# Kernel optimization log

Measured on AMD Instinct MI355X. Metric: run time of the kernel, lower is better.

## Reference

```python
import jax, jax.numpy as jnp
import numpy as np

N_NODES = 100000
N_EDGES = 800000
IN_FEATS = 128
NUM_CLASSES = 64


def setup_inputs() -> dict:
    key = jax.random.key(0)
    k1, k2, k3, k4 = jax.random.split(key, 4)
    x = jax.random.normal(k1, (N_NODES, IN_FEATS), dtype=jnp.float32)
    edge_src = jax.random.randint(k2, (N_EDGES,), 0, N_NODES, dtype=jnp.int64)
    edge_dst = jax.random.randint(k3, (N_EDGES,), 0, N_NODES, dtype=jnp.int64)
    W_neigh = jax.random.normal(k4, (NUM_CLASSES, IN_FEATS), dtype=jnp.float32) * (1.0 / np.sqrt(IN_FEATS))
    b_neigh = jnp.zeros((NUM_CLASSES,), dtype=jnp.float32)
    return {"x": x, "edge_src": edge_src, "edge_dst": edge_dst,
            "W_neigh": W_neigh, "b_neigh": b_neigh}


def reference(x, edge_src, edge_dst, W_neigh, b_neigh):
    # DGL SAGEConv with aggregator_type='gcn':
    #   h_neigh[v] = (sum_{u->v} x[u] + x[v]) / (in_degree(v) + 1)
    #   out = h_neigh @ W_neigh^T + b_neigh
    n = x.shape[0]
    # gather source features per edge, scatter-sum into destinations
    neigh_sum = jax.ops.segment_sum(x[edge_src], edge_dst, num_segments=n)  # [N, F]
    deg = jax.ops.segment_sum(jnp.ones((edge_src.shape[0],), dtype=x.dtype),
                              edge_dst, num_segments=n)                     # [N]
    h = (neigh_sum + x) / (deg + 1.0)[:, None]
    out = jnp.einsum('nf,cf->nc', h, W_neigh) + b_neigh
    return out
```

## Files before the change

### kernel.cpp

```cpp
#include <hip/hip_runtime.h>

#define N_NODES 100000
#define N_EDGES 800000
#define IN_FEATS 128
#define NUM_CLASSES 64

#define NSB    98
#define SCAP   9216
#define BINCAP 56
#define NBKT   12500
#define NBKT_PAD (NSB * 128)
#define HCAP   88
#define BKCAP  176

#define K1_GRID 1955

typedef short bf16x8 __attribute__((ext_vector_type(8)));
typedef float f32x4  __attribute__((ext_vector_type(4)));

static __device__ __forceinline__ unsigned short f2bf(float f) {
    unsigned u = __float_as_uint(f);
    unsigned r = (u + 0x7fffu + ((u >> 16) & 1u)) >> 16;
    return (unsigned short)r;
}
static __device__ __forceinline__ float bf2f(unsigned short v) {
    return __uint_as_float(((unsigned)v) << 16);
}

static __device__ __forceinline__ void gemm_body(char* smem, int gid,
                                                 const float* __restrict__ x,
                                                 const float* __restrict__ W,
                                                 unsigned short* __restrict__ y16) {
    const long base = (long)gid * 64;
    if (base >= N_NODES) return;

    unsigned short* Wf = (unsigned short*)smem;
    typedef unsigned short XsRow[136];
    XsRow* Xs = (XsRow*)(smem + 16384);

    const int tid = threadIdx.x;

    for (int i = tid; i < 4 * 4 * 64 * 8; i += 256) {
        const int j    = i & 7;
        const int lane = (i >> 3) & 63;
        const int t    = (i >> 9) & 3;
        const int s    = i >> 11;
        const int k = s * 32 + ((lane >> 4) << 3) + j;
        const int c = t * 16 + (lane & 15);
        Wf[i] = f2bf(W[c * IN_FEATS + k]);
    }

#pragma unroll
    for (int it = 0; it < 8; ++it) {
        const int i   = tid + it * 256;
        const int row = i >> 5;
        const int c4  = (i & 31) << 2;
        const long node = base + row;
        float4 v = make_float4(0.f, 0.f, 0.f, 0.f);
        if (node < N_NODES) v = *(const float4*)&x[node * IN_FEATS + c4];
        ushort4 w4;
        w4.x = f2bf(v.x); w4.y = f2bf(v.y); w4.z = f2bf(v.z); w4.w = f2bf(v.w);
        *(ushort4*)&Xs[row][c4] = w4;
    }
    __syncthreads();

    const int wave = tid >> 6;
    const int lane = tid & 63;
    const long nb  = base + wave * 16;

    bf16x8 wf[4][4];
#pragma unroll
    for (int s = 0; s < 4; ++s)
#pragma unroll
        for (int t = 0; t < 4; ++t)
            wf[s][t] = *(const bf16x8*)&Wf[(((s * 4 + t) * 64) + lane) * 8];

    f32x4 acc[4];
#pragma unroll
    for (int t = 0; t < 4; ++t) acc[t] = (f32x4){0.f, 0.f, 0.f, 0.f};

    const int m  = lane & 15;
    const int kq = lane >> 4;
    const unsigned short* arow = &Xs[wave * 16 + m][kq * 8];

#pragma unroll
    for (int s = 0; s < 4; ++s) {
        bf16x8 af = *(const bf16x8*)(arow + s * 32);
#pragma unroll
        for (int t = 0; t < 4; ++t)
            acc[t] = __builtin_amdgcn_mfma_f32_16x16x32_bf16(af, wf[s][t], acc[t], 0, 0, 0);
    }

    const int ccol  = lane & 15;
    const int rbase = (lane >> 4) << 2;
#pragma unroll
    for (int t = 0; t < 4; ++t) {
#pragma unroll
        for (int r = 0; r < 4; ++r) {
            const long n2 = nb + rbase + r;
            if (n2 < N_NODES)
                y16[n2 * NUM_CLASSES + t * 16 + ccol] = f2bf(acc[t][r]);
        }
    }
}

static __device__ __forceinline__ void p1_body(char* smem, int p1id,
                                               const int* __restrict__ esrc,
                                               const int* __restrict__ edst,
                                               int* __restrict__ sbcur,
                                               unsigned* __restrict__ stage) {
    typedef unsigned BinRow[BINCAP];
    BinRow* bins = (BinRow*)smem;
    int* bcnt  = (int*)(smem + 21952);
    int* bbase = (int*)(smem + 21952 + 392);

    const int tid = threadIdx.x;
    for (int i = tid; i < NSB; i += 256) bcnt[i] = 0;
    __syncthreads();

    const int e0 = p1id * 2048;
#pragma unroll
    for (int it = 0; it < 8; ++it) {
        const int e = e0 + it * 256 + tid;
        if (e < N_EDGES) {
            const unsigned s  = (unsigned)esrc[e];
            const unsigned d  = (unsigned)edst[e];
            const unsigned sb = d >> 10;
            const unsigned pk = s | ((d & 1023u) << 17);
            const int p = atomicAdd(&bcnt[sb], 1);
            if (p < BINCAP) {
                bins[sb][p] = pk;
            } else {
                const int gp = atomicAdd(&sbcur[sb << 4], 1);
                if (gp < SCAP) stage[sb * SCAP + gp] = pk;
            }
        }
    }
    __syncthreads();

    if (tid < NSB) {
        const int c = min(bcnt[tid], BINCAP);
        bcnt[tid]  = c;
        bbase[tid] = atomicAdd(&sbcur[tid << 4], c);
    }
    __syncthreads();

    for (int i = tid; i < NSB * BINCAP; i += 256) {
        const int sb = i / BINCAP;
        const int k  = i - sb * BINCAP;
        if (k < bcnt[sb]) {
            const int pos = bbase[sb] + k;
            if (pos < SCAP) stage[sb * SCAP + pos] = bins[sb][k];
        }
    }
}

__global__ __launch_bounds__(256) void k1_gemm_scatter(const float* __restrict__ x,
                                                       const float* __restrict__ W,
                                                       unsigned short* __restrict__ y16,
                                                       const int* __restrict__ esrc,
                                                       const int* __restrict__ edst,
                                                       int* __restrict__ sbcur,
                                                       unsigned* __restrict__ stage) {
    __shared__ __align__(16) char smem[33792];
    const int bid = blockIdx.x;
    const int r   = bid % 5;
    if (r == 4) {
        p1_body(smem, bid / 5, esrc, edst, sbcur, stage);
    } else {
        gemm_body(smem, (bid / 5) * 4 + r, x, W, y16);
    }
}

__global__ __launch_bounds__(256) void scatter_p2(const unsigned* __restrict__ stage,
                                                  const int* __restrict__ sbcur,
                                                  unsigned* __restrict__ pairs,
                                                  int* __restrict__ cnt_g) {
    __shared__ int lcnt[128];
    const int sb  = blockIdx.x >> 1;
    const int h   = blockIdx.x & 1;
    const int tid = threadIdx.x;

    if (tid < 128) lcnt[tid] = 0;
    __syncthreads();

    const int ecnt = min(sbcur[sb << 4], SCAP);
    const int half = (ecnt + 1) >> 1;
    const int lo   = h * half;
    const int hi   = min(ecnt, lo + half);

    const unsigned* sp = stage + (size_t)sb * SCAP;
    unsigned* pp = pairs + (size_t)sb * 128 * BKCAP + h * HCAP;

    for (int i = lo + tid; i < hi; i += 256) {
        const unsigned pk   = sp[i];
        const unsigned dlow = pk >> 17;
        const int fb = (int)(dlow >> 3);
        const unsigned dl = dlow & 7u;
        const int r = atomicAdd(&lcnt[fb], 1);
        if (r < HCAP) pp[fb * BKCAP + r] = (pk & 0x1FFFFu) | (dl << 20);
    }
    __syncthreads();

    if (tid < 128) cnt_g[((sb << 7) + tid) * 2 + h] = min(lcnt[tid], HCAP);
}

__global__ __launch_bounds__(256) void gather_bucket(const unsigned short* __restrict__ y16,
                                                     const unsigned* __restrict__ pairs,
                                                     const int* __restrict__ cnt_g,
                                                     const float* __restrict__ b,
                                                     float* __restrict__ out) {
    __shared__ float slab[4][8][64];
    __shared__ int   cnt[4][8];

    const int tid  = threadIdx.x;
    const int wave = tid >> 6;
    const int lane = tid & 63;
    const int bkt  = blockIdx.x;

    {
        float4* sz = (float4*)&slab[0][0][0];
        sz[tid]       = make_float4(0.f, 0.f, 0.f, 0.f);
        sz[tid + 256] = make_float4(0.f, 0.f, 0.f, 0.f);
    }

    const int half = wave >> 1;
    const int ws   = wave & 1;
    const int mh = cnt_g[bkt * 2 + half];
    const int q  = (mh + 1) >> 1;
    const int s0 = ws * q;
    const int s1 = min(mh, s0 + q);
    const int m  = max(0, s1 - s0);

    const unsigned* pb = pairs + (size_t)bkt * BKCAP + half * HCAP + s0;
    unsigned pr = 0;
    if (lane < m) pr = pb[lane];

    unsigned long long cnt64 = 0;
    __syncthreads();

    int j = 0;
    for (; j + 4 <= m; j += 4) {
        const unsigned p0 = __shfl(pr, j);
        const unsigned p1 = __shfl(pr, j + 1);
        const unsigned p2 = __shfl(pr, j + 2);
        const unsigned p3 = __shfl(pr, j + 3);
        const float v0 = bf2f(y16[(size_t)(p0 & 0xFFFFFu) * NUM_CLASSES + lane]);
        const float v1 = bf2f(y16[(size_t)(p1 & 0xFFFFFu) * NUM_CLASSES + lane]);
        const float v2 = bf2f(y16[(size_t)(p2 & 0xFFFFFu) * NUM_CLASSES + lane]);
        const float v3 = bf2f(y16[(size_t)(p3 & 0xFFFFFu) * NUM_CLASSES + lane]);
        slab[wave][p0 >> 20][lane] += v0;
        slab[wave][p1 >> 20][lane] += v1;
        slab[wave][p2 >> 20][lane] += v2;
        slab[wave][p3 >> 20][lane] += v3;
        cnt64 += (1ull << ((p0 >> 20) * 8)) + (1ull << ((p1 >> 20) * 8))
               + (1ull << ((p2 >> 20) * 8)) + (1ull << ((p3 >> 20) * 8));
    }
    for (; j < m; ++j) {
        const unsigned p = __shfl(pr, j);
        slab[wave][p >> 20][lane] += bf2f(y16[(size_t)(p & 0xFFFFFu) * NUM_CLASSES + lane]);
        cnt64 += 1ull << ((p >> 20) * 8);
    }

    if (lane < 8) cnt[wave][lane] = (int)((cnt64 >> (lane * 8)) & 0xFFull);
    __syncthreads();

    const int c = tid & 63;
#pragma unroll
    for (int i = 0; i < 2; ++i) {
        const int n = (tid >> 6) + 4 * i;
        const size_t v = ((size_t)bkt << 3) + n;
        const float s = slab[0][n][c] + slab[1][n][c] + slab[2][n][c] + slab[3][n][c];
        const int  dg = cnt[0][n] + cnt[1][n] + cnt[2][n] + cnt[3][n];
        const float self = bf2f(y16[v * NUM_CLASSES + c]);
        out[v * NUM_CLASSES + c] = (s + self) / (float)(dg + 1) + b[c];
    }
}

extern "C" void kernel_launch(void* const* d_in, const int* in_sizes, int n_in,
                              void* d_out, int out_size, void* d_ws, size_t ws_size,
                              hipStream_t stream) {
    const float* x    = (const float*)d_in[0];
    const int*   esrc = (const int*)d_in[1];
    const int*   edst = (const int*)d_in[2];
    const float* W    = (const float*)d_in[3];
    const float* b    = (const float*)d_in[4];
    float* out = (float*)d_out;

    char* p = (char*)d_ws;
    unsigned short* y16 = (unsigned short*)p;  p += (size_t)N_NODES * NUM_CLASSES * 2;
    unsigned* stage     = (unsigned*)p;        p += (size_t)NSB * SCAP * 4;
    unsigned* pairs     = (unsigned*)p;        p += (size_t)NBKT * BKCAP * 4;
    int* cnt_g          = (int*)p;             p += (size_t)NBKT_PAD * 2 * 4;
    int* sbcur          = (int*)p;             p += (size_t)NSB * 16 * 4;

    hipMemsetAsync(sbcur, 0, (size_t)NSB * 16 * 4, stream);

    k1_gemm_scatter<<<K1_GRID, 256, 0, stream>>>(x, W, y16, esrc, edst, sbcur, stage);

    scatter_p2<<<NSB * 2, 256, 0, stream>>>(stage, sbcur, pairs, cnt_g);

    gather_bucket<<<NBKT, 256, 0, stream>>>(y16, pairs, cnt_g, b, out);
}
```

Before: 156.0 us.

## Sort edges by destination node within buckets and gather per node with registers

The second scatter pass becomes a count-then-place counting sort. Edges within each 8-node bucket are grouped by exact destination node, with per-node counts and offsets, and the grid grows to four blocks per superblock. The gather kernel now gives one wave per bucket and accumulates each node's neighbours in registers using readlane indices. This removes the shared-memory slab accumulation, the barriers and the packed degree counters. The cost is that scatter_p2 reads the stage buffer twice, and any bucket with more than 128 edges is silently truncated.

```diff
diff --git a/kernel.cpp b/kernel.cpp
--- a/kernel.cpp
+++ b/kernel.cpp
@@ -10,8 +10,7 @@
 #define BINCAP 56
 #define NBKT   12500
 #define NBKT_PAD (NSB * 128)
-#define HCAP   88
-#define BKCAP  176
+#define PB_CAP 128
 
 #define K1_GRID 1955
 
@@ -176,104 +175,97 @@
                                                   const int* __restrict__ sbcur,
                                                   unsigned* __restrict__ pairs,
                                                   int* __restrict__ cnt_g) {
-    __shared__ int lcnt[128];
-    const int sb  = blockIdx.x >> 1;
-    const int h   = blockIdx.x & 1;
+    __shared__ int lcnt[256];
+    __shared__ int loff[256];
+    const int sb  = blockIdx.x >> 2;
+    const int q   = blockIdx.x & 3;
     const int tid = threadIdx.x;
 
-    if (tid < 128) lcnt[tid] = 0;
+    lcnt[tid] = 0;
     __syncthreads();
 
     const int ecnt = min(sbcur[sb << 4], SCAP);
-    const int half = (ecnt + 1) >> 1;
-    const int lo   = h * half;
-    const int hi   = min(ecnt, lo + half);
-
     const unsigned* sp = stage + (size_t)sb * SCAP;
-    unsigned* pp = pairs + (size_t)sb * 128 * BKCAP + h * HCAP;
-
-    for (int i = lo + tid; i < hi; i += 256) {
+
+    for (int i = tid; i < ecnt; i += 256) {
         const unsigned pk   = sp[i];
         const unsigned dlow = pk >> 17;
-        const int fb = (int)(dlow >> 3);
-        const unsigned dl = dlow & 7u;
-        const int r = atomicAdd(&lcnt[fb], 1);
-        if (r < HCAP) pp[fb * BKCAP + r] = (pk & 0x1FFFFu) | (dl << 20);
-    }
-    __syncthreads();
-
-    if (tid < 128) cnt_g[((sb << 7) + tid) * 2 + h] = min(lcnt[tid], HCAP);
-}
-
-__global__ __launch_bounds__(256) void gather_bucket(const unsigned short* __restrict__ y16,
-                                                     const unsigned* __restrict__ pairs,
-                                                     const int* __restrict__ cnt_g,
-                                                     const float* __restrict__ b,
-                                                     float* __restrict__ out) {
-    __shared__ float slab[4][8][64];
-    __shared__ int   cnt[4][8];
-
+        const unsigned fb   = dlow >> 3;
+        if ((fb & 3u) == (unsigned)q)
+            atomicAdd(&lcnt[(int)(((fb >> 2) << 3) + (dlow & 7u))], 1);
+    }
+    __syncthreads();
+
+    if (tid < 32) {
+        const int fb     = (tid << 2) + q;
+        const int gnode0 = (sb << 10) + (fb << 3);
+        int run = 0;
+#pragma unroll
+        for (int k = 0; k < 8; ++k) {
+            const int li = (tid << 3) + k;
+            const int c  = lcnt[li];
+            const int st = min(run, PB_CAP);
+            const int en = min(run + c, PB_CAP);
+            loff[li] = st;
+            cnt_g[gnode0 + k] = en - st;
+            run += c;
+        }
+    }
+    __syncthreads();
+
+    for (int i = tid; i < ecnt; i += 256) {
+        const unsigned pk   = sp[i];
+        const unsigned dlow = pk >> 17;
+        const unsigned fb   = dlow >> 3;
+        if ((fb & 3u) == (unsigned)q) {
+            const int li = (int)(((fb >> 2) << 3) + (dlow & 7u));
+            const int r  = atomicAdd(&loff[li], 1);
+            if (r < PB_CAP)
+                pairs[((size_t)(sb << 7) + fb) * PB_CAP + r] = pk & 0x1FFFFu;
+        }
+    }
+}
+
+__global__ __launch_bounds__(256) void gather_node(const unsigned short* __restrict__ y16,
+                                                   const unsigned* __restrict__ pairs,
+                                                   const int* __restrict__ cnt_g,
+                                                   const float* __restrict__ b,
+                                                   float* __restrict__ out) {
     const int tid  = threadIdx.x;
     const int wave = tid >> 6;
     const int lane = tid & 63;
-    const int bkt  = blockIdx.x;
-
-    {
-        float4* sz = (float4*)&slab[0][0][0];
-        sz[tid]       = make_float4(0.f, 0.f, 0.f, 0.f);
-        sz[tid + 256] = make_float4(0.f, 0.f, 0.f, 0.f);
-    }
-
-    const int half = wave >> 1;
-    const int ws   = wave & 1;
-    const int mh = cnt_g[bkt * 2 + half];
-    const int q  = (mh + 1) >> 1;
-    const int s0 = ws * q;
-    const int s1 = min(mh, s0 + q);
-    const int m  = max(0, s1 - s0);
-
-    const unsigned* pb = pairs + (size_t)bkt * BKCAP + half * HCAP + s0;
-    unsigned pr = 0;
-    if (lane < m) pr = pb[lane];
-
-    unsigned long long cnt64 = 0;
-    __syncthreads();
-
-    int j = 0;
-    for (; j + 4 <= m; j += 4) {
-        const unsigned p0 = __shfl(pr, j);
-        const unsigned p1 = __shfl(pr, j + 1);
-        const unsigned p2 = __shfl(pr, j + 2);
-        const unsigned p3 = __shfl(pr, j + 3);
-        const float v0 = bf2f(y16[(size_t)(p0 & 0xFFFFFu) * NUM_CLASSES + lane]);
-        const float v1 = bf2f(y16[(size_t)(p1 & 0xFFFFFu) * NUM_CLASSES + lane]);
-        const float v2 = bf2f(y16[(size_t)(p2 & 0xFFFFFu) * NUM_CLASSES + lane]);
-        const float v3 = bf2f(y16[(size_t)(p3 & 0xFFFFFu) * NUM_CLASSES + lane]);
-        slab[wave][p0 >> 20][lane] += v0;
-        slab[wave][p1 >> 20][lane] += v1;
-        slab[wave][p2 >> 20][lane] += v2;
-        slab[wave][p3 >> 20][lane] += v3;
-        cnt64 += (1ull << ((p0 >> 20) * 8)) + (1ull << ((p1 >> 20) * 8))
-               + (1ull << ((p2 >> 20) * 8)) + (1ull << ((p3 >> 20) * 8));
-    }
-    for (; j < m; ++j) {
-        const unsigned p = __shfl(pr, j);
-        slab[wave][p >> 20][lane] += bf2f(y16[(size_t)(p & 0xFFFFFu) * NUM_CLASSES + lane]);
-        cnt64 += 1ull << ((p >> 20) * 8);
-    }
-
-    if (lane < 8) cnt[wave][lane] = (int)((cnt64 >> (lane * 8)) & 0xFFull);
-    __syncthreads();
-
-    const int c = tid & 63;
-#pragma unroll
-    for (int i = 0; i < 2; ++i) {
-        const int n = (tid >> 6) + 4 * i;
-        const size_t v = ((size_t)bkt << 3) + n;
-        const float s = slab[0][n][c] + slab[1][n][c] + slab[2][n][c] + slab[3][n][c];
-        const int  dg = cnt[0][n] + cnt[1][n] + cnt[2][n] + cnt[3][n];
-        const float self = bf2f(y16[v * NUM_CLASSES + c]);
-        out[v * NUM_CLASSES + c] = (s + self) / (float)(dg + 1) + b[c];
+    const int bkt  = blockIdx.x * 4 + wave;
+    const int g0   = bkt << 3;
+
+    const unsigned* pb = pairs + (size_t)bkt * PB_CAP;
+    const int r0 = (int)pb[lane];
+    const int r1 = (int)pb[64 + lane];
+    int cc = 0;
+    if (lane < 8) cc = cnt_g[g0 + lane];
+    const float bl = b[lane];
+
+    int off = 0;
+#pragma unroll
+    for (int n = 0; n < 8; ++n) {
+        const int c = __builtin_amdgcn_readlane(cc, n);
+        float acc = 0.f;
+        const int e0 = min(c, max(0, 64 - off));
+        const int s1 = off + e0 - 64;
+        const int e1 = c - e0;
+#pragma unroll 4
+        for (int j = 0; j < e0; ++j) {
+            const unsigned p = (unsigned)__builtin_amdgcn_readlane(r0, off + j);
+            acc += bf2f(y16[(size_t)p * NUM_CLASSES + lane]);
+        }
+#pragma unroll 4
+        for (int j = 0; j < e1; ++j) {
+            const unsigned p = (unsigned)__builtin_amdgcn_readlane(r1, s1 + j);
+            acc += bf2f(y16[(size_t)p * NUM_CLASSES + lane]);
+        }
+        off += c;
+        const size_t v = (size_t)(g0 + n);
+        const float self = bf2f(y16[v * NUM_CLASSES + lane]);
+        out[v * NUM_CLASSES + lane] = (acc + self) / (float)(c + 1) + bl;
     }
 }
 
@@ -290,15 +282,15 @@
     char* p = (char*)d_ws;
     unsigned short* y16 = (unsigned short*)p;  p += (size_t)N_NODES * NUM_CLASSES * 2;
     unsigned* stage     = (unsigned*)p;        p += (size_t)NSB * SCAP * 4;
-    unsigned* pairs     = (unsigned*)p;        p += (size_t)NBKT * BKCAP * 4;
-    int* cnt_g          = (int*)p;             p += (size_t)NBKT_PAD * 2 * 4;
+    unsigned* pairs     = (unsigned*)p;        p += (size_t)NBKT_PAD * PB_CAP * 4;
+    int* cnt_g          = (int*)p;             p += (size_t)NBKT_PAD * 8 * 4;
     int* sbcur          = (int*)p;             p += (size_t)NSB * 16 * 4;
 
     hipMemsetAsync(sbcur, 0, (size_t)NSB * 16 * 4, stream);
 
     k1_gemm_scatter<<<K1_GRID, 256, 0, stream>>>(x, W, y16, esrc, edst, sbcur, stage);
 
-    scatter_p2<<<NSB * 2, 256, 0, stream>>>(stage, sbcur, pairs, cnt_g);
-
-    gather_bucket<<<NBKT, 256, 0, stream>>>(y16, pairs, cnt_g, b, out);
-}
+    scatter_p2<<<NSB * 4, 256, 0, stream>>>(stage, sbcur, pairs, cnt_g);
+
+    gather_node<<<NBKT / 4, 256, 0, stream>>>(y16, pairs, cnt_g, b, out);
+}
```

Result: slower. 192.6 us (+23.5%).
